# Kernel optimization log

Measured on AMD Instinct MI355X. Metric: run time of the kernel, lower is better.

## Reference

```python
import jax, jax.numpy as jnp
import numpy as np

D_MODEL = 1024
D_KV = 64
N_HEADS = 16
KV_HEADS = 4
G = N_HEADS // KV_HEADS
NUM_BUCKETS = 32
MAX_DISTANCE = 128


def _relative_position_bucket(relative_position, bidirectional=True,
                              num_buckets=NUM_BUCKETS, max_distance=MAX_DISTANCE):
    # Faithful port of T5Attention._relative_position_bucket
    relative_buckets = jnp.zeros_like(relative_position)
    if bidirectional:
        num_buckets //= 2
        relative_buckets = (relative_position > 0).astype(jnp.int32) * num_buckets
        relative_position = jnp.abs(relative_position)
    else:
        relative_position = -jnp.minimum(relative_position, 0)
    max_exact = num_buckets // 2
    is_small = relative_position < max_exact
    rel_if_large = max_exact + (
        jnp.log(relative_position.astype(jnp.float32) / max_exact)
        / np.log(max_distance / max_exact) * (num_buckets - max_exact)
    ).astype(jnp.int32)
    rel_if_large = jnp.minimum(rel_if_large, num_buckets - 1)
    return relative_buckets + jnp.where(is_small, relative_position, rel_if_large)


def setup_inputs() -> dict:
    key = jax.random.key(0)
    ks = jax.random.split(key, 6)
    B, S = 2, 2048
    inner = N_HEADS * D_KV
    sc = 1.0 / np.sqrt(D_MODEL)
    return {
        "hidden_states": jax.random.normal(ks[0], (B, S, D_MODEL), dtype=jnp.float32),
        "Wq": jax.random.normal(ks[1], (D_MODEL, inner), dtype=jnp.float32) * sc,
        "Wk": jax.random.normal(ks[2], (D_MODEL, inner), dtype=jnp.float32) * sc,
        "Wv": jax.random.normal(ks[3], (D_MODEL, inner), dtype=jnp.float32) * sc,
        "Wo": jax.random.normal(ks[4], (inner, D_MODEL), dtype=jnp.float32) * sc,
        "rel_bias": jax.random.normal(ks[5], (NUM_BUCKETS, N_HEADS), dtype=jnp.float32) * 0.1,
    }


def reference(hidden_states, Wq, Wk, Wv, Wo, rel_bias):
    B, S, _ = hidden_states.shape

    def split_heads(x):  # [B,S,inner] -> [B,H,S,Dk]
        return x.reshape(B, S, N_HEADS, D_KV).transpose(0, 2, 1, 3)

    q = split_heads(hidden_states @ Wq)
    k = split_heads(hidden_states @ Wk)
    v = split_heads(hidden_states @ Wv)

    # head index = g * KV_HEADS + h (einops 'b (g h) ...' with h=kv_heads)
    gq = q.reshape(B, G, KV_HEADS, S, D_KV)
    gk = k.reshape(B, G, KV_HEADS, S, D_KV).mean(axis=1)  # [B,Hkv,S,Dk]
    # einsum sums over g (as in torch.einsum 'bghnd,bhsd->bhns'); no 1/sqrt(d) in T5
    scores = jnp.einsum('bghnd,bhsd->bhns', gq, gk)  # [B,Hkv,S,S]

    # T5 relative position bias (bidirectional, encoder)
    ctx = jnp.arange(S)[:, None]
    mem = jnp.arange(S)[None, :]
    buckets = _relative_position_bucket(mem - ctx, bidirectional=True)
    bias = rel_bias[buckets]                # [S,S,H]
    bias = bias.transpose(2, 0, 1)[None]    # [1,H,S,S]
    gbias = bias.reshape(1, G, KV_HEADS, S, S).mean(axis=1)  # [1,Hkv,S,S]

    scores = scores + gbias
    attn = jax.nn.softmax(scores.astype(jnp.float32), axis=-1).astype(scores.dtype)

    # repeat grouped attn weights back to full heads: 'b h n s -> b (g h) n s'
    attn_full = jnp.tile(attn, (1, G, 1, 1))  # [B,H,S,S]
    ctx_out = jnp.einsum('bhns,bhsd->bhnd', attn_full, v)  # [B,H,S,Dk]
    ctx_out = ctx_out.transpose(0, 2, 1, 3).reshape(B, S, N_HEADS * D_KV)
    return ctx_out @ Wo  # [B,S,D_MODEL]
```

## Files before the change

### kernel.cpp

```cpp
#include <hip/hip_runtime.h>
#include <math.h>


typedef __bf16 bf16_t;
typedef bf16_t bf16x8 __attribute__((ext_vector_type(8)));
typedef bf16_t bf16x4 __attribute__((ext_vector_type(4)));
typedef float f32x4 __attribute__((ext_vector_type(4)));

#define MFMA16(a, b, c) __builtin_amdgcn_mfma_f32_16x16x32_bf16(a, b, c, 0, 0, 0)

typedef __attribute__((address_space(1))) void gvoid;
typedef __attribute__((address_space(3))) void svoid;
__device__ __forceinline__ void gld16(const void* g, void* l) {
    __builtin_amdgcn_global_load_lds((gvoid*)g, (svoid*)l, 16, 0, 0);
}

__global__ __launch_bounds__(256) void prep_all(const float* __restrict__ hs,
                                                const float* __restrict__ Wq,
                                                const float* __restrict__ Wk,
                                                const float* __restrict__ Wv,
                                                const float* __restrict__ Wo,
                                                const float* __restrict__ rel_bias,
                                                bf16_t* __restrict__ hs_hi,
                                                bf16_t* __restrict__ hs_lo,
                                                bf16_t* __restrict__ Thi,
                                                bf16_t* __restrict__ Tlo,
                                                bf16_t* __restrict__ WvT,
                                                bf16_t* __restrict__ WoT,
                                                float* __restrict__ btab) {
    __shared__ float sm[2048];
    const int r = blockIdx.x, t = threadIdx.x;
    if (r < 4096) {
        size_t idx = ((size_t)r * 256 + t) * 4;
        float4 v = *(const float4*)(hs + idx);
        bf16x4 h, l;
        h[0] = (bf16_t)v.x; l[0] = (bf16_t)(v.x - (float)h[0]);
        h[1] = (bf16_t)v.y; l[1] = (bf16_t)(v.y - (float)h[1]);
        h[2] = (bf16_t)v.z; l[2] = (bf16_t)(v.z - (float)h[2]);
        h[3] = (bf16_t)v.w; l[3] = (bf16_t)(v.w - (float)h[3]);
        *(bf16x4*)(hs_hi + idx) = h;
        *(bf16x4*)(hs_lo + idx) = l;
    } else if (r < 5120) {
        int k = r - 4096;
        float* rq = sm;
        float* rk = sm + 1024;
#pragma unroll
        for (int j = 0; j < 4; ++j) {
            rq[t + j * 256] = Wq[(size_t)k * 1024 + t + j * 256];
            rk[t + j * 256] = Wk[(size_t)k * 1024 + t + j * 256];
        }
        __syncthreads();
        int h = t >> 6, j2 = t & 63;
        float sq = 0.f, sk = 0.f;
#pragma unroll
        for (int g = 0; g < 4; ++g) {
            sq += rq[(g * 4 + h) * 64 + j2];
            sk += rk[(g * 4 + h) * 64 + j2];
        }
        sk *= 0.25f;
        bf16_t qh = (bf16_t)sq;
        Thi[(size_t)t * 1024 + k] = qh;
        Tlo[(size_t)t * 1024 + k] = (bf16_t)(sq - (float)qh);
        bf16_t kh = (bf16_t)sk;
        Thi[(size_t)(256 + t) * 1024 + k] = kh;
        Tlo[(size_t)(256 + t) * 1024 + k] = (bf16_t)(sk - (float)kh);
    } else if (r < 7168) {
        const float* src = (r < 6144) ? Wv : Wo;
        bf16_t* dst = (r < 6144) ? WvT : WoT;
        int rr = (r < 6144) ? r - 5120 : r - 6144;
        int bx = (rr & 31) * 32, by = (rr >> 5) * 32;
        int tx = t & 31, ty = t >> 5;
        float(*tile)[33] = (float(*)[33])sm;
#pragma unroll
        for (int i = 0; i < 32; i += 8)
            tile[ty + i][tx] = src[(size_t)(by + ty + i) * 1024 + bx + tx];
        __syncthreads();
#pragma unroll
        for (int i = 0; i < 32; i += 8)
            dst[(size_t)(bx + ty + i) * 1024 + by + tx] = (bf16_t)tile[tx][ty + i];
    } else {
        int idx = (r - 7168) * 256 + t;
        if (idx >= 4095) return;
        int delta = idx - 2047;
        int bucket = (delta > 0) ? 16 : 0;
        int arp = delta < 0 ? -delta : delta;
        int rb;
        if (arp < 8) {
            rb = arp;
        } else {
            float tt = (logf((float)arp * 0.125f) / 2.772588722239781f) * 8.0f;
            int ri = 8 + (int)tt;
            rb = ri < 15 ? ri : 15;
        }
        bucket += rb;
#pragma unroll
        for (int h = 0; h < 4; ++h) {
            float s = 0.25f * (rel_bias[bucket * 16 + h] + rel_bias[bucket * 16 + h + 4] +
                               rel_bias[bucket * 16 + h + 8] + rel_bias[bucket * 16 + h + 12]);
            btab[h * 4608 + idx] = s;
        }
    }
}

__global__ __launch_bounds__(256, 1) void proj_qkv(const bf16_t* __restrict__ Ah,
                                                   const bf16_t* __restrict__ Al,
                                                   const bf16_t* __restrict__ Bh,
                                                   const bf16_t* __restrict__ Bl,
                                                   const bf16_t* __restrict__ WvT,
                                                   bf16_t* __restrict__ Qhi,
                                                   bf16_t* __restrict__ Qlo,
                                                   bf16_t* __restrict__ Kbh,
                                                   bf16_t* __restrict__ Kbl,
                                                   bf16_t* __restrict__ Vb) {
    __shared__ bf16_t pool[36864];
    const int K = 1024, nk = 32;
    const int t = threadIdx.x;
    const int w = t >> 6, lane = t & 63;
    const int lr = lane & 15, q = lane >> 4;
    const int bx = blockIdx.x;
    const bool qk = bx < 8;
    const int m0 = blockIdx.y * 128;
    const int n0 = qk ? bx * 64 : (bx - 8) * 128;
    const int mw = (w & 1) * 64;
    f32x4 acc[4][4] = {};

    const int rA = t & 127, cA0 = t >> 7, cA1 = 2 + (t >> 7);
    const size_t oA0 = (size_t)(m0 + rA) * K + cA0 * 8;
    const size_t oA1 = (size_t)(m0 + rA) * K + cA1 * 8;
    const int rBq = t & 63, cBq = t >> 6;
    const size_t oBq = (size_t)(n0 + rBq) * K + cBq * 8;
    const size_t oBv0 = (size_t)(n0 + rA) * K + cA0 * 8;
    const size_t oBv1 = (size_t)(n0 + rA) * K + cA1 * 8;

    auto stage = [&](int bf, int kidx) {
        const int k0 = kidx * 32;
        bf16_t* base = &pool[bf * 12288];
        gld16(Ah + oA0 + k0, base + t * 8);
        gld16(Ah + oA1 + k0, base + (256 + t) * 8);
        if (qk) {
            gld16(Al + oA0 + k0, base + 4096 + t * 8);
            gld16(Al + oA1 + k0, base + 4096 + (256 + t) * 8);
            gld16(Bh + oBq + k0, base + 8192 + t * 8);
            gld16(Bl + oBq + k0, base + 10240 + t * 8);
        } else {
            gld16(WvT + oBv0 + k0, base + 4096 + t * 8);
            gld16(WvT + oBv1 + k0, base + 4096 + (256 + t) * 8);
        }
    };

    stage(0, 0);
    stage(1, 1);
    stage(2, 2);
    if (qk)
        asm volatile("s_waitcnt vmcnt(12)" ::: "memory");
    else
        asm volatile("s_waitcnt vmcnt(8)" ::: "memory");
    __builtin_amdgcn_s_barrier();

    for (int it = 0; it < nk; ++it) {
        const int cur = it % 3;
        const bf16_t* base = &pool[cur * 12288];
        if (qk) {
            const int nw = (w >> 1) * 32;
            bf16x8 ah[4], al[4], bh[2], bl[2];
#pragma unroll
            for (int i = 0; i < 4; ++i) {
                int sa = (q * 128 + mw + i * 16 + lr) * 8;
                ah[i] = *(const bf16x8*)&base[sa];
                al[i] = *(const bf16x8*)&base[4096 + sa];
            }
#pragma unroll
            for (int j = 0; j < 2; ++j) {
                int sb = (q * 64 + nw + j * 16 + lr) * 8;
                bh[j] = *(const bf16x8*)&base[8192 + sb];
                bl[j] = *(const bf16x8*)&base[10240 + sb];
            }
            asm volatile("s_waitcnt lgkmcnt(0)" ::: "memory");
            if (it + 2 < nk)
                asm volatile("s_waitcnt vmcnt(6)" ::: "memory");
            else
                asm volatile("s_waitcnt vmcnt(0)" ::: "memory");
            __builtin_amdgcn_s_barrier();
            if (it + 3 < nk) stage(cur, it + 3);
            __builtin_amdgcn_sched_barrier(0);
#pragma unroll
            for (int i = 0; i < 4; ++i)
#pragma unroll
                for (int j = 0; j < 2; ++j) {
                    acc[i][j] = MFMA16(ah[i], bh[j], acc[i][j]);
                    acc[i][j] = MFMA16(ah[i], bl[j], acc[i][j]);
                    acc[i][j] = MFMA16(al[i], bh[j], acc[i][j]);
                }
        } else {
            const int nw = (w >> 1) * 64;
            bf16x8 af[4], bfv[4];
#pragma unroll
            for (int i = 0; i < 4; ++i)
                af[i] = *(const bf16x8*)&base[(q * 128 + mw + i * 16 + lr) * 8];
#pragma unroll
            for (int j = 0; j < 4; ++j)
                bfv[j] = *(const bf16x8*)&base[4096 + (q * 128 + nw + j * 16 + lr) * 8];
            asm volatile("s_waitcnt lgkmcnt(0)" ::: "memory");
            if (it + 2 < nk)
                asm volatile("s_waitcnt vmcnt(4)" ::: "memory");
            else
                asm volatile("s_waitcnt vmcnt(0)" ::: "memory");
            __builtin_amdgcn_s_barrier();
            if (it + 3 < nk) stage(cur, it + 3);
            __builtin_amdgcn_sched_barrier(0);
#pragma unroll
            for (int i = 0; i < 4; ++i)
#pragma unroll
                for (int j = 0; j < 4; ++j) acc[i][j] = MFMA16(af[i], bfv[j], acc[i][j]);
        }
    }

    const int nj = qk ? 2 : 4;
    const int nwq = qk ? (w >> 1) * 32 : (w >> 1) * 64;
#pragma unroll
    for (int i = 0; i < 4; ++i) {
        int row = m0 + mw + i * 16 + q * 4;
#pragma unroll 4
        for (int j = 0; j < nj; ++j) {
            int col = n0 + nwq + j * 16 + lr;
#pragma unroll
            for (int reg = 0; reg < 4; ++reg) {
                float x = acc[i][j][reg];
                int token = row + reg;
                if (qk) {
                    bf16_t hi = (bf16_t)x;
                    bf16_t lo = (bf16_t)(x - (float)hi);
                    if (col < 256) {
                        size_t o = (size_t)token * 256 + col;
                        Qhi[o] = hi;
                        Qlo[o] = lo;
                    } else {
                        int hc = col - 256;
                        int h = hc >> 6, d = hc & 63;
                        int b = token >> 11, s = token & 2047;
                        int it2 = s >> 6, sl = s & 63;
                        size_t o = ((size_t)((b * 4 + h) * 32 + it2)) * 4096 +
                                   (size_t)((d >> 3) * 64 + sl) * 8 + (d & 7);
                        Kbh[o] = hi;
                        Kbl[o] = lo;
                    }
                } else {
                    int vg = col;
                    int h = (vg >> 6) & 3, g = vg >> 8, d = vg & 63;
                    int b = token >> 11, s = token & 2047;
                    int it2 = s >> 6, sc = (s >> 3) & 7, si = s & 7;
                    size_t o = ((size_t)((b * 4 + h) * 32 + it2)) * 16384 +
                               (size_t)(sc * 256 + g * 64 + d) * 8 + si;
                    Vb[o] = (bf16_t)x;
                }
            }
        }
    }
}

__global__ __launch_bounds__(256, 1) void gemm_out(const bf16_t* __restrict__ A,
                                                   const bf16_t* __restrict__ BT,
                                                   float* __restrict__ C,
                                                   int M, int N, int K) {
    __shared__ bf16_t pool[18432];
    const int t = threadIdx.x;
    const int w = t >> 6, lane = t & 63;
    const int lr = lane & 15, q = lane >> 4;
    const int m0 = blockIdx.y * 128, n0 = blockIdx.x * 64;
    const int mw = (w & 1) * 64, nw = (w >> 1) * 32;
    f32x4 acc[4][2] = {};
    const int nk = K >> 5;

    const int rA = t & 127, cA0 = t >> 7, cA1 = 2 + (t >> 7);
    const bf16_t* gA0 = A + (size_t)(m0 + rA) * K + cA0 * 8;
    const bf16_t* gA1 = A + (size_t)(m0 + rA) * K + cA1 * 8;
    const bf16_t* gB = BT + (size_t)(n0 + (t & 63)) * K + (t >> 6) * 8;

    auto stage = [&](int bf, int kidx) {
        const int k0 = kidx * 32;
        bf16_t* base = &pool[bf * 6144];
        gld16(gA0 + k0, base + t * 8);
        gld16(gA1 + k0, base + (256 + t) * 8);
        gld16(gB + k0, base + 4096 + t * 8);
    };

    stage(0, 0);
    stage(1, 1);
    stage(2, 2);
    asm volatile("s_waitcnt vmcnt(6)" ::: "memory");
    __builtin_amdgcn_s_barrier();

    for (int it = 0; it < nk; ++it) {
        const int cur = it % 3;
        const bf16_t* base = &pool[cur * 6144];
        bf16x8 af[4], bfv[2];
#pragma unroll
        for (int i = 0; i < 4; ++i)
            af[i] = *(const bf16x8*)&base[(q * 128 + mw + i * 16 + lr) * 8];
#pragma unroll
        for (int j = 0; j < 2; ++j)
            bfv[j] = *(const bf16x8*)&base[4096 + (q * 64 + nw + j * 16 + lr) * 8];
        asm volatile("s_waitcnt lgkmcnt(0)" ::: "memory");
        if (it + 2 < nk)
            asm volatile("s_waitcnt vmcnt(3)" ::: "memory");
        else
            asm volatile("s_waitcnt vmcnt(0)" ::: "memory");
        __builtin_amdgcn_s_barrier();
        if (it + 3 < nk) stage(cur, it + 3);
        __builtin_amdgcn_sched_barrier(0);
#pragma unroll
        for (int i = 0; i < 4; ++i)
#pragma unroll
            for (int j = 0; j < 2; ++j) acc[i][j] = MFMA16(af[i], bfv[j], acc[i][j]);
    }

#pragma unroll
    for (int i = 0; i < 4; ++i) {
        int row = m0 + mw + i * 16 + q * 4;
#pragma unroll
        for (int j = 0; j < 2; ++j) {
            int col = n0 + nw + j * 16 + lr;
#pragma unroll
            for (int reg = 0; reg < 4; ++reg)
                C[(size_t)(row + reg) * N + col] = acc[i][j][reg];
        }
    }
}

__global__ __launch_bounds__(512, 1) void attn_mfma(const bf16_t* __restrict__ Qhi,
                                                    const bf16_t* __restrict__ Qlo,
                                                    const bf16_t* __restrict__ Kbh,
                                                    const bf16_t* __restrict__ Kbl,
                                                    const bf16_t* __restrict__ Vb,
                                                    const float* __restrict__ btab,
                                                    bf16_t* __restrict__ part0,
                                                    bf16_t* __restrict__ part1,
                                                    float* __restrict__ Sml) {
    __shared__ bf16_t Kh[2][4096], Kl[2][4096], Vsm[2][16384], Ps[8192];
    const int t = threadIdx.x, w = t >> 6, lane = t & 63;
    const int lr = lane & 15, q = lane >> 4;
    const int blk = blockIdx.x;
    const int half = blk & 1, qt = (blk >> 1) & 15, h = (blk >> 5) & 3, b = blk >> 7;
    const int n0 = qt * 128;
    const int rowbase = n0 + w * 16;
    const int swz = (lr & 7) << 3;
    const int psb = w * 1024 + lr * 64;

    const size_t qrow = (size_t)(b * 2048 + rowbase + lr) * 256 + h * 64;
    bf16x8 aqh[2], aql[2];
#pragma unroll
    for (int kb = 0; kb < 2; ++kb) {
        aqh[kb] = *(const bf16x8*)(Qhi + qrow + kb * 32 + q * 8);
        aql[kb] = *(const bf16x8*)(Qlo + qrow + kb * 32 + q * 8);
    }

    const int tilebase = (b * 4 + h) * 32 + half * 16;
    const bf16_t* gK = Kbh + (size_t)tilebase * 4096;
    const bf16_t* gL = Kbl + (size_t)tilebase * 4096;
    const bf16_t* gV = Vb + (size_t)tilebase * 16384;
    const float* btabh = btab + h * 4608 + 2047;

    auto stage = [&](int bf, int it) {
        gld16(gK + (size_t)it * 4096 + t * 8, &Kh[bf][t * 8]);
        gld16(gL + (size_t)it * 4096 + t * 8, &Kl[bf][t * 8]);
        const bf16_t* v0 = gV + (size_t)it * 16384;
#pragma unroll
        for (int j = 0; j < 4; ++j)
            gld16(v0 + (j * 512 + t) * 8, &Vsm[bf][(j * 512 + t) * 8]);
    };

    float m_r = -INFINITY, l_r = 0.f;
    f32x4 O[16] = {};

    stage(0, 0);
    __syncthreads();
    for (int it = 0; it < 16; ++it) {
        const int cur = it & 1;
        if (it + 1 < 16) stage(cur ^ 1, it + 1);
        const int s0g = half * 1024 + it * 64;

        f32x4 sc[4];
#pragma unroll
        for (int ct = 0; ct < 4; ++ct) {
            f32x4 z = {0.f, 0.f, 0.f, 0.f};
#pragma unroll
            for (int kb = 0; kb < 2; ++kb) {
                int sb = ((kb * 4 + q) * 64 + ct * 16 + lr) * 8;
                bf16x8 bh = *(const bf16x8*)&Kh[cur][sb];
                bf16x8 bl = *(const bf16x8*)&Kl[cur][sb];
                z = MFMA16(bh, aqh[kb], z);
                z = MFMA16(bh, aql[kb], z);
                z = MFMA16(bl, aqh[kb], z);
            }
            sc[ct] = z;
        }
        const int dbase = (s0g + q * 4) - (rowbase + lr);
#pragma unroll
        for (int ct = 0; ct < 4; ++ct)
#pragma unroll
            for (int reg = 0; reg < 4; ++reg)
                sc[ct][reg] += btabh[dbase + ct * 16 + reg];

        float mt = fmaxf(fmaxf(sc[0][0], sc[0][1]), fmaxf(sc[0][2], sc[0][3]));
#pragma unroll
        for (int ct = 1; ct < 4; ++ct)
            mt = fmaxf(mt, fmaxf(fmaxf(sc[ct][0], sc[ct][1]), fmaxf(sc[ct][2], sc[ct][3])));
        mt = fmaxf(mt, __shfl_xor(mt, 16, 64));
        mt = fmaxf(mt, __shfl_xor(mt, 32, 64));

        float mn = fmaxf(m_r, mt);
        float al = __expf(m_r - mn);
        m_r = mn;
        float rs = 0.f;
#pragma unroll
        for (int ct = 0; ct < 4; ++ct) {
            bf16x4 tq;
#pragma unroll
            for (int reg = 0; reg < 4; ++reg) {
                float p = __expf(sc[ct][reg] - mn);
                rs += p;
                tq[reg] = (bf16_t)p;
            }
            *(bf16x4*)&Ps[psb + ((ct * 16 + q * 4) ^ swz)] = tq;
        }
        rs += __shfl_xor(rs, 16, 64);
        rs += __shfl_xor(rs, 32, 64);
        l_r = l_r * al + rs;

        bf16x8 pf0 = *(const bf16x8*)&Ps[psb + ((q * 8) ^ swz)];
        bf16x8 pf1 = *(const bf16x8*)&Ps[psb + ((32 + q * 8) ^ swz)];

#pragma unroll
        for (int nt = 0; nt < 16; ++nt) {
            f32x4 o = O[nt];
#pragma unroll
            for (int reg = 0; reg < 4; ++reg) o[reg] *= al;
            bf16x8 v0 = *(const bf16x8*)&Vsm[cur][(q * 256 + nt * 16 + lr) * 8];
            o = MFMA16(v0, pf0, o);
            bf16x8 v1 = *(const bf16x8*)&Vsm[cur][((4 + q) * 256 + nt * 16 + lr) * 8];
            o = MFMA16(v1, pf1, o);
            O[nt] = o;
        }
        __syncthreads();
    }

    bf16_t* P = half ? part1 : part0;
    const float inv = 1.f / l_r;
    const int tokb = b * 2048 + rowbase;
#pragma unroll
    for (int G = 0; G < 4; ++G) {
#pragma unroll
        for (int g4 = 0; g4 < 4; ++g4) {
            int nt = G * 4 + g4;
            bf16x4 tq;
#pragma unroll
            for (int reg = 0; reg < 4; ++reg) tq[reg] = (bf16_t)(O[nt][reg] * inv);
            *(bf16x4*)&Ps[psb + ((g4 * 16 + q * 4) ^ swz)] = tq;
        }
#pragma unroll
        for (int i = 0; i < 2; ++i) {
            int row = i * 8 + (lane >> 3), cv = (lane & 7) * 8;
            bf16x8 fr = *(const bf16x8*)&Ps[w * 1024 + row * 64 + (cv ^ ((row & 7) << 3))];
            *(bf16x8*)(P + (size_t)(tokb + row) * 1024 + (G * 4 + h) * 64 + cv) = fr;
        }
    }
    if (lane < 16)
        Sml[half * 16384 + (size_t)(tokb + lane) * 4 + h] = m_r + logf(l_r);
}

__global__ __launch_bounds__(256) void combine_halves(bf16_t* __restrict__ p0,
                                                      const bf16_t* __restrict__ p1,
                                                      const float* __restrict__ Sml) {
    size_t flat = ((size_t)blockIdx.x * 256 + threadIdx.x) * 8;
    int tok = (int)(flat >> 10), c = (int)(flat & 1023), h = (c >> 6) & 3;
    float s0 = Sml[tok * 4 + h], s1 = Sml[16384 + tok * 4 + h];
    float M = fmaxf(s0, s1);
    float e0 = __expf(s0 - M), e1 = __expf(s1 - M);
    float r = 1.f / (e0 + e1);
    float w0 = e0 * r, w1 = e1 * r;
    bf16x8 a = *(bf16x8*)(p0 + flat);
    bf16x8 bb = *(const bf16x8*)(p1 + flat);
    bf16x8 o;
#pragma unroll
    for (int i = 0; i < 8; ++i) o[i] = (bf16_t)(w0 * (float)a[i] + w1 * (float)bb[i]);
    *(bf16x8*)(p0 + flat) = o;
}

extern "C" void kernel_launch(void* const* d_in, const int* in_sizes, int n_in,
                              void* d_out, int out_size, void* d_ws, size_t ws_size,
                              hipStream_t stream) {
    const float* hs = (const float*)d_in[0];
    const float* Wq = (const float*)d_in[1];
    const float* Wk = (const float*)d_in[2];
    const float* Wv = (const float*)d_in[3];
    const float* Wo = (const float*)d_in[4];
    const float* rb = (const float*)d_in[5];
    float* out = (float*)d_out;

    const size_t MB = 1 << 20;
    const size_t KB = 1 << 10;
    char* ws = (char*)d_ws;
    bf16_t* hs_hi = (bf16_t*)(ws);
    bf16_t* hs_lo = (bf16_t*)(ws + 8 * MB);
    bf16_t* WqkThi = (bf16_t*)(ws + 16 * MB);
    bf16_t* WqkTlo = (bf16_t*)(ws + 17 * MB);
    bf16_t* WvT = (bf16_t*)(ws + 18 * MB);
    bf16_t* WoT = (bf16_t*)(ws + 20 * MB);
    float* btab = (float*)(ws + 22 * MB);
    float* Sml = (float*)(ws + 22 * MB + 128 * KB);
    bf16_t* Qhi = (bf16_t*)(ws + 22 * MB + 256 * KB);
    bf16_t* Qlo = Qhi + (size_t)4096 * 256;
    bf16_t* Kbh = Qlo + (size_t)4096 * 256;
    bf16_t* Kbl = Kbh + (size_t)4096 * 256;
    bf16_t* Vb = Kbl + (size_t)4096 * 256;
    bf16_t* part0 = hs_hi;
    bf16_t* part1 = hs_lo;

    prep_all<<<7184, 256, 0, stream>>>(hs, Wq, Wk, Wv, Wo, rb, hs_hi, hs_lo, WqkThi,
                                       WqkTlo, WvT, WoT, btab);
    proj_qkv<<<dim3(16, 32), 256, 0, stream>>>(hs_hi, hs_lo, WqkThi, WqkTlo, WvT, Qhi,
                                               Qlo, Kbh, Kbl, Vb);
    attn_mfma<<<256, 512, 0, stream>>>(Qhi, Qlo, Kbh, Kbl, Vb, btab, part0, part1, Sml);
    combine_halves<<<2048, 256, 0, stream>>>(part0, part1, Sml);
    gemm_out<<<dim3(16, 32), 256, 0, stream>>>(part0, WoT, out, 4096, 1024, 1024);
}
```

Before: 243.8 us.

## Remap block indices for XCD locality and vectorize V projection stores

Block indices in the QKV projection, output GEMM and attention kernels are permuted so consecutive hardware block IDs (round-robined across XCDs) map to neighbouring tiles, aiming to improve per-XCD L2 reuse of shared operands. The V-projection epilogue is split from the Q/K path and writes four bf16 values per vector store instead of scalar stores. The modulo buffer index becomes a rotating counter, and the sched_barrier after staging is removed, letting the compiler interleave loads with MFMAs, which risks reordering relative to the manual waitcnt scheme.

```diff
diff --git a/kernel.cpp b/kernel.cpp
--- a/kernel.cpp
+++ b/kernel.cpp
@@ -117,9 +117,11 @@
     const int t = threadIdx.x;
     const int w = t >> 6, lane = t & 63;
     const int lr = lane & 15, q = lane >> 4;
-    const int bx = blockIdx.x;
+    const int l = blockIdx.y * 16 + blockIdx.x;
+    const int nl = (l & 7) * 64 + (l >> 3);
+    const int bx = nl & 15;
+    const int m0 = (nl >> 4) * 128;
     const bool qk = bx < 8;
-    const int m0 = blockIdx.y * 128;
     const int n0 = qk ? bx * 64 : (bx - 8) * 128;
     const int mw = (w & 1) * 64;
     f32x4 acc[4][4] = {};
@@ -133,8 +135,8 @@
     const size_t oBv1 = (size_t)(n0 + rA) * K + cA1 * 8;
 
     auto stage = [&](int bf, int kidx) {
+        bf16_t* base = &pool[bf * 12288];
         const int k0 = kidx * 32;
-        bf16_t* base = &pool[bf * 12288];
         gld16(Ah + oA0 + k0, base + t * 8);
         gld16(Ah + oA1 + k0, base + (256 + t) * 8);
         if (qk) {
@@ -157,8 +159,8 @@
         asm volatile("s_waitcnt vmcnt(8)" ::: "memory");
     __builtin_amdgcn_s_barrier();
 
+    int cur = 0;
     for (int it = 0; it < nk; ++it) {
-        const int cur = it % 3;
         const bf16_t* base = &pool[cur * 12288];
         if (qk) {
             const int nw = (w >> 1) * 32;
@@ -176,13 +178,12 @@
                 bl[j] = *(const bf16x8*)&base[10240 + sb];
             }
             asm volatile("s_waitcnt lgkmcnt(0)" ::: "memory");
-            if (it + 2 < nk)
+            if (it < nk - 2)
                 asm volatile("s_waitcnt vmcnt(6)" ::: "memory");
             else
                 asm volatile("s_waitcnt vmcnt(0)" ::: "memory");
             __builtin_amdgcn_s_barrier();
             if (it + 3 < nk) stage(cur, it + 3);
-            __builtin_amdgcn_sched_barrier(0);
 #pragma unroll
             for (int i = 0; i < 4; ++i)
 #pragma unroll
@@ -201,33 +202,32 @@
             for (int j = 0; j < 4; ++j)
                 bfv[j] = *(const bf16x8*)&base[4096 + (q * 128 + nw + j * 16 + lr) * 8];
             asm volatile("s_waitcnt lgkmcnt(0)" ::: "memory");
-            if (it + 2 < nk)
+            if (it < nk - 2)
                 asm volatile("s_waitcnt vmcnt(4)" ::: "memory");
             else
                 asm volatile("s_waitcnt vmcnt(0)" ::: "memory");
             __builtin_amdgcn_s_barrier();
             if (it + 3 < nk) stage(cur, it + 3);
-            __builtin_amdgcn_sched_barrier(0);
 #pragma unroll
             for (int i = 0; i < 4; ++i)
 #pragma unroll
                 for (int j = 0; j < 4; ++j) acc[i][j] = MFMA16(af[i], bfv[j], acc[i][j]);
         }
-    }
-
-    const int nj = qk ? 2 : 4;
-    const int nwq = qk ? (w >> 1) * 32 : (w >> 1) * 64;
-#pragma unroll
-    for (int i = 0; i < 4; ++i) {
-        int row = m0 + mw + i * 16 + q * 4;
-#pragma unroll 4
-        for (int j = 0; j < nj; ++j) {
-            int col = n0 + nwq + j * 16 + lr;
-#pragma unroll
-            for (int reg = 0; reg < 4; ++reg) {
-                float x = acc[i][j][reg];
-                int token = row + reg;
-                if (qk) {
+        cur = (cur == 2) ? 0 : cur + 1;
+    }
+
+    if (qk) {
+        const int nwq = (w >> 1) * 32;
+#pragma unroll
+        for (int i = 0; i < 4; ++i) {
+            int row = m0 + mw + i * 16 + q * 4;
+#pragma unroll
+            for (int j = 0; j < 2; ++j) {
+                int col = n0 + nwq + j * 16 + lr;
+#pragma unroll
+                for (int reg = 0; reg < 4; ++reg) {
+                    float x = acc[i][j][reg];
+                    int token = row + reg;
                     bf16_t hi = (bf16_t)x;
                     bf16_t lo = (bf16_t)(x - (float)hi);
                     if (col < 256) {
@@ -236,23 +236,34 @@
                         Qlo[o] = lo;
                     } else {
                         int hc = col - 256;
-                        int h = hc >> 6, d = hc & 63;
+                        int hh = hc >> 6, d = hc & 63;
                         int b = token >> 11, s = token & 2047;
                         int it2 = s >> 6, sl = s & 63;
-                        size_t o = ((size_t)((b * 4 + h) * 32 + it2)) * 4096 +
+                        size_t o = ((size_t)((b * 4 + hh) * 32 + it2)) * 4096 +
                                    (size_t)((d >> 3) * 64 + sl) * 8 + (d & 7);
                         Kbh[o] = hi;
                         Kbl[o] = lo;
                     }
-                } else {
-                    int vg = col;
-                    int h = (vg >> 6) & 3, g = vg >> 8, d = vg & 63;
-                    int b = token >> 11, s = token & 2047;
-                    int it2 = s >> 6, sc = (s >> 3) & 7, si = s & 7;
-                    size_t o = ((size_t)((b * 4 + h) * 32 + it2)) * 16384 +
-                               (size_t)(sc * 256 + g * 64 + d) * 8 + si;
-                    Vb[o] = (bf16_t)x;
                 }
+            }
+        }
+    } else {
+        const int nwq = (w >> 1) * 64;
+#pragma unroll
+        for (int i = 0; i < 4; ++i) {
+            int row = m0 + mw + i * 16 + q * 4;
+            int b = row >> 11, s = row & 2047;
+            int it2 = s >> 6, sc2 = (s >> 3) & 7, si = s & 7;
+#pragma unroll
+            for (int j = 0; j < 4; ++j) {
+                int col = n0 + nwq + j * 16 + lr;
+                int hh = (col >> 6) & 3, g = col >> 8, d = col & 63;
+                size_t o = ((size_t)((b * 4 + hh) * 32 + it2)) * 16384 +
+                           (size_t)(sc2 * 256 + g * 64 + d) * 8 + si;
+                bf16x4 pv;
+#pragma unroll
+                for (int reg = 0; reg < 4; ++reg) pv[reg] = (bf16_t)acc[i][j][reg];
+                *(bf16x4*)(Vb + o) = pv;
             }
         }
     }
@@ -266,7 +277,9 @@
     const int t = threadIdx.x;
     const int w = t >> 6, lane = t & 63;
     const int lr = lane & 15, q = lane >> 4;
-    const int m0 = blockIdx.y * 128, n0 = blockIdx.x * 64;
+    const int l = blockIdx.y * 16 + blockIdx.x;
+    const int nl = (l & 7) * 64 + (l >> 3);
+    const int m0 = (nl >> 4) * 128, n0 = (nl & 15) * 64;
     const int mw = (w & 1) * 64, nw = (w >> 1) * 32;
     f32x4 acc[4][2] = {};
     const int nk = K >> 5;
@@ -277,8 +290,8 @@
     const bf16_t* gB = BT + (size_t)(n0 + (t & 63)) * K + (t >> 6) * 8;
 
     auto stage = [&](int bf, int kidx) {
+        bf16_t* base = &pool[bf * 6144];
         const int k0 = kidx * 32;
-        bf16_t* base = &pool[bf * 6144];
         gld16(gA0 + k0, base + t * 8);
         gld16(gA1 + k0, base + (256 + t) * 8);
         gld16(gB + k0, base + 4096 + t * 8);
@@ -290,8 +303,8 @@
     asm volatile("s_waitcnt vmcnt(6)" ::: "memory");
     __builtin_amdgcn_s_barrier();
 
+    int cur = 0;
     for (int it = 0; it < nk; ++it) {
-        const int cur = it % 3;
         const bf16_t* base = &pool[cur * 6144];
         bf16x8 af[4], bfv[2];
 #pragma unroll
@@ -301,17 +314,17 @@
         for (int j = 0; j < 2; ++j)
             bfv[j] = *(const bf16x8*)&base[4096 + (q * 64 + nw + j * 16 + lr) * 8];
         asm volatile("s_waitcnt lgkmcnt(0)" ::: "memory");
-        if (it + 2 < nk)
+        if (it < nk - 2)
             asm volatile("s_waitcnt vmcnt(3)" ::: "memory");
         else
             asm volatile("s_waitcnt vmcnt(0)" ::: "memory");
         __builtin_amdgcn_s_barrier();
         if (it + 3 < nk) stage(cur, it + 3);
-        __builtin_amdgcn_sched_barrier(0);
 #pragma unroll
         for (int i = 0; i < 4; ++i)
 #pragma unroll
             for (int j = 0; j < 2; ++j) acc[i][j] = MFMA16(af[i], bfv[j], acc[i][j]);
+        cur = (cur == 2) ? 0 : cur + 1;
     }
 
 #pragma unroll
@@ -339,7 +352,8 @@
     __shared__ bf16_t Kh[2][4096], Kl[2][4096], Vsm[2][16384], Ps[8192];
     const int t = threadIdx.x, w = t >> 6, lane = t & 63;
     const int lr = lane & 15, q = lane >> 4;
-    const int blk = blockIdx.x;
+    const int bl0 = blockIdx.x;
+    const int blk = (bl0 & 7) * 32 + (bl0 >> 3);
     const int half = blk & 1, qt = (blk >> 1) & 15, h = (blk >> 5) & 3, b = blk >> 7;
     const int n0 = qt * 128;
     const int rowbase = n0 + w * 16;
```

New measurement: 220.9 us. -9.4%, faster.
